# Optimization experiments

Measured on AMD Instinct MI355X. Metric: run time of the kernel, lower is better.

## Reference

```python
import jax, jax.numpy as jnp
import numpy as np

B, S, E, H = 8, 3072, 512, 8  # batch, total seq (3 chunks of 1024), emb_size, num_heads


def setup_inputs() -> dict:
    key = jax.random.key(0)
    ks = jax.random.split(key, 9)
    sc = 0.02  # weight init scale
    return {
        "x": jax.random.normal(ks[0], (B, S, E), jnp.float32),
        "Wq": jax.random.normal(ks[1], (3, E, E), jnp.float32) * sc,
        "bq": jax.random.normal(ks[2], (3, E), jnp.float32) * sc,
        "Wk": jax.random.normal(ks[3], (3, E, E), jnp.float32) * sc,
        "bk": jax.random.normal(ks[4], (3, E), jnp.float32) * sc,
        "Wv": jax.random.normal(ks[5], (3, E, E), jnp.float32) * sc,
        "bv": jax.random.normal(ks[6], (3, E), jnp.float32) * sc,
        "Wp": jax.random.normal(ks[7], (3, E, E), jnp.float32) * sc,
        "bp": jax.random.normal(ks[8], (3, E), jnp.float32) * sc,
    }


def reference(x, Wq, bq, Wk, bk, Wv, bv, Wp, bp):
    b, s, e = x.shape
    d = e // H
    # split into 3 chunks along seq: xc[c] is chunk c, shape [b, n, e]
    xc = jnp.stack(jnp.split(x, 3, axis=1))  # [3, b, n, e]

    def lin(W, bias):  # torch Linear: x @ W.T + b, per chunk
        return jnp.einsum('cbne,cfe->cbnf', xc, W) + bias[:, None, None, :]

    def heads(t):  # [3, b, n, e] -> [3, b, h, n, d]
        c, bb, n, _ = t.shape
        return t.reshape(c, bb, n, H, d).transpose(0, 1, 3, 2, 4)

    q = heads(lin(Wq, bq))
    k = heads(lin(Wk, bk))
    v = heads(lin(Wv, bv))

    # rotated cross-chunk pairing (faithful to source):
    # out1 = attn(q2, k3, v3); out2 = attn(q3, k1, v1); out3 = attn(q1, k2, v2)
    q_sel = q[jnp.array([1, 2, 0])]
    k_sel = k[jnp.array([2, 0, 1])]
    v_sel = v[jnp.array([2, 0, 1])]

    scaling = jnp.sqrt(jnp.float32(e))  # note: sqrt(emb_size), not sqrt(head_dim)
    energy = jnp.einsum('cbhqd,cbhkd->cbhqk', q_sel, k_sel) / scaling
    att = jax.nn.softmax(energy, axis=-1)  # dropout: eval-mode identity
    out = jnp.einsum('cbhqk,cbhkd->cbhqd', att, v_sel)
    out = out.transpose(0, 1, 3, 2, 4).reshape(3, b, s // 3, e)  # merge heads
    out = jnp.einsum('cbne,cfe->cbnf', out, Wp) + bp[:, None, None, :]
    return jnp.concatenate([out[0], out[1], out[2]], axis=1)  # [b, s, e]
```

## Files before the change

### kernel.cpp

```cpp
#include <hip/hip_runtime.h>
#include <hip/hip_bf16.h>


typedef __attribute__((ext_vector_type(8))) short short8v;
typedef __attribute__((ext_vector_type(4))) float float4v;
typedef __attribute__((ext_vector_type(4))) unsigned short ushort4v;
typedef __attribute__((ext_vector_type(4))) unsigned int uint4v;

#define CHUNKS 3
#define BATCH 8
#define SEQ 3072
#define EMB 512
#define NH 8
#define HD 64
#define NCK 1024
#define MTOT (BATCH*SEQ)
#define QKV_ELEMS (CHUNKS*BATCH*NH*NCK*HD)
#define WELEMS (CHUNKS*EMB*EMB)
#define QSCALE 0.06375872465f

__device__ __forceinline__ unsigned short f2b(float f) {
  union { float f; unsigned int i; } x; x.f = f;
  unsigned int r = x.i + 0x7FFFu + ((x.i >> 16) & 1u);
  return (unsigned short)(r >> 16);
}
__device__ __forceinline__ unsigned int pack2r(float a, float b) {
  union { float f; unsigned int u; } xa, xb; xa.f = a; xb.f = b;
  return __builtin_amdgcn_perm(xb.u + 0x8000u, xa.u + 0x8000u, 0x07060302u);
}
__device__ __forceinline__ void gld_lds16(const unsigned short* g, unsigned short* l) {
  __builtin_amdgcn_global_load_lds(
      (const __attribute__((address_space(1))) unsigned int*)g,
      (__attribute__((address_space(3))) unsigned int*)l, 16, 0, 0);
}
#define MFMA(a, b, c) __builtin_amdgcn_mfma_f32_16x16x32_bf16(a, b, c, 0, 0, 0)

__global__ __launch_bounds__(256) void conv_x(
    const float* __restrict__ src, unsigned short* __restrict__ dst)
{
  size_t i = ((size_t)blockIdx.x * 256 + threadIdx.x) * 8;
  float4 a = *(const float4*)&src[i];
  float4 b = *(const float4*)&src[i + 4];
  uint4v p;
  p[0] = pack2r(a.x, a.y); p[1] = pack2r(a.z, a.w);
  p[2] = pack2r(b.x, b.y); p[3] = pack2r(b.z, b.w);
  *(uint4v*)&dst[i] = p;
}

__global__ __launch_bounds__(256) void conv_w(
    const float* __restrict__ s0, const float* __restrict__ s1,
    const float* __restrict__ s2, const float* __restrict__ s3,
    unsigned short* __restrict__ dst)
{
  const int z = blockIdx.y;
  const float* s = (z == 0) ? s0 : (z == 1) ? s1 : (z == 2) ? s2 : s3;
  size_t i = ((size_t)blockIdx.x * 256 + threadIdx.x) * 8;
  float4 a = *(const float4*)&s[i];
  float4 b = *(const float4*)&s[i + 4];
  uint4v p;
  p[0] = pack2r(a.x, a.y); p[1] = pack2r(a.z, a.w);
  p[2] = pack2r(b.x, b.y); p[3] = pack2r(b.z, b.w);
  *(uint4v*)&dst[(size_t)z * WELEMS + i] = p;
}

__global__ __launch_bounds__(256) void qkv_gemm(
    const unsigned short* __restrict__ xb, const unsigned short* __restrict__ Wb,
    const float* __restrict__ bq, const float* __restrict__ bk,
    const float* __restrict__ bv,
    unsigned short* __restrict__ qt, unsigned short* __restrict__ kt,
    unsigned short* __restrict__ vt)
{
  const int tid = threadIdx.x;
  const int w = tid >> 6, l = tid & 63;
  const int ln = l & 15, qu = l >> 4;
  const int sr = l >> 3, kbl = l & 7;
  const int bid = blockIdx.x;
  const int lin = (bid & 7) * 288 + (bid >> 3);
  const int col0 = (lin & 3) * 128;
  const int z = (lin >> 2) % 3;
  const int row0 = (lin / 12) * 128;
  const int bglob = row0 / SEQ;
  const int c = (row0 % SEQ) / NCK;
  const int n0 = row0 % NCK;
  const unsigned short* W = Wb + (size_t)z * WELEMS + c * EMB * EMB;
  const float* bias = (z == 0 ? bq : (z == 1 ? bk : bv)) + c * EMB;
  const float oscale = (z == 0) ? QSCALE : 1.0f;

  __shared__ unsigned short As[128 * 64];
  __shared__ unsigned short Bs[128 * 64];

  const int xo = (w & 1) * 64, fo = (w >> 1) * 64;

  float4v acc[4][4];
#pragma unroll
  for (int i = 0; i < 4; ++i)
#pragma unroll
    for (int j = 0; j < 4; ++j) acc[i][j] = (float4v){0.f, 0.f, 0.f, 0.f};

  for (int k0 = 0; k0 < EMB; k0 += 64) {
    __syncthreads();
#pragma unroll
    for (int s = 0; s < 4; ++s) {
      int rbase = w * 32 + s * 8;
      int r = rbase + sr;
      int kb_g = kbl ^ sr;
      gld_lds16(&xb[(size_t)(row0 + r) * EMB + k0 + kb_g * 8], &As[rbase * 64]);
      gld_lds16(&W [(size_t)(col0 + r) * EMB + k0 + kb_g * 8], &Bs[rbase * 64]);
    }
    __syncthreads();
#pragma unroll
    for (int ks = 0; ks < 2; ++ks) {
      short8v xf[4], wf[4];
#pragma unroll
      for (int i = 0; i < 4; ++i) {
        int rx = xo + 16 * i + ln;
        xf[i] = *(const short8v*)&As[rx * 64 + (((ks * 4 + qu) ^ (rx & 7)) * 8)];
        int rw = fo + 16 * i + ln;
        wf[i] = *(const short8v*)&Bs[rw * 64 + (((ks * 4 + qu) ^ (rw & 7)) * 8)];
      }
      if (z <= 1) {
#pragma unroll
        for (int i = 0; i < 4; ++i)
#pragma unroll
          for (int j = 0; j < 4; ++j) acc[i][j] = MFMA(wf[j], xf[i], acc[i][j]);
      } else {
#pragma unroll
        for (int i = 0; i < 4; ++i)
#pragma unroll
          for (int j = 0; j < 4; ++j) acc[i][j] = MFMA(xf[i], wf[j], acc[i][j]);
      }
    }
  }

  if (z <= 1) {
    unsigned short* outp = (z == 0) ? qt : kt;
#pragma unroll
    for (int j = 0; j < 4; ++j) {
      int f0 = col0 + fo + 16 * j + 4 * qu;
      float4 b4 = *(const float4*)&bias[f0];
      int hh = f0 >> 6, dd0 = f0 & 63;
      size_t base = ((size_t)((c * 8 + bglob) * 8 + hh)) << 16;
#pragma unroll
      for (int i = 0; i < 4; ++i) {
        int n = n0 + xo + 16 * i + ln;
        ushort4v p;
#pragma unroll
        for (int r = 0; r < 4; ++r)
          p[r] = f2b((acc[i][j][r] + ((const float*)&b4)[r]) * oscale);
        *(ushort4v*)&outp[base + (size_t)n * 64 + dd0] = p;
      }
    }
  } else {
#pragma unroll
    for (int i = 0; i < 4; ++i) {
      int nn0 = n0 + xo + 16 * i + 4 * qu;
#pragma unroll
      for (int j = 0; j < 4; ++j) {
        int f = col0 + fo + 16 * j + ln;
        int hh = f >> 6, dd = f & 63;
        float bvv = bias[f];
        size_t base = ((size_t)((c * 8 + bglob) * 8 + hh)) << 16;
        ushort4v p;
#pragma unroll
        for (int r = 0; r < 4; ++r) p[r] = f2b(acc[i][j][r] + bvv);
        *(ushort4v*)&vt[base + (size_t)dd * 1024 + nn0] = p;
      }
    }
  }
}

#define ATTN_STAGE(buf, kt0v) do {                                             \
  int r = w * 8;                                                               \
  gld_lds16(&Kg[(size_t)((kt0v) + r + sr) * 64 + ((kbl ^ sr) * 8)],            \
            &Ks[buf][r * 64]);                                                 \
  gld_lds16(&Vg[(size_t)(r + sr) * 1024 + (kt0v) + ((kbl ^ sr) * 8)],          \
            &Vs[buf][r * 64]);                                                 \
} while (0)

__global__ __launch_bounds__(512) void attn_kernel(
    const unsigned short* __restrict__ qt,
    const unsigned short* __restrict__ kt,
    const unsigned short* __restrict__ vt,
    unsigned short* __restrict__ attnb)
{
  const int tid = threadIdx.x;
  const int w = tid >> 6, l = tid & 63;
  const int ln = l & 15, qu = l >> 4;
  const int sr = l >> 3, kbl = l & 7;
  const int bid = blockIdx.x;
  const int hd = bid % 192;
  const int q0 = (bid / 192) * 256;
  const int co = hd >> 6;
  const int b  = (hd >> 3) & 7;
  const int h  = hd & 7;
  const int cq = (co + 1) % 3, ckv = (co + 2) % 3;
  const unsigned short* Qg = qt + ((size_t)((cq  * 8 + b) * 8 + h) << 16);
  const unsigned short* Kg = kt + ((size_t)((ckv * 8 + b) * 8 + h) << 16);
  const unsigned short* Vg = vt + ((size_t)((ckv * 8 + b) * 8 + h) << 16);

  __shared__ unsigned short Ks[2][64 * 64];
  __shared__ unsigned short Vs[2][64 * 64];

  short8v qf[2][2];
#pragma unroll
  for (int nt = 0; nt < 2; ++nt)
#pragma unroll
    for (int ks = 0; ks < 2; ++ks)
      qf[nt][ks] = *(const short8v*)&Qg[(size_t)(q0 + w * 32 + nt * 16 + ln) * 64 + ks * 32 + qu * 8];

  short8v onesf;
#pragma unroll
  for (int i = 0; i < 8; ++i) onesf[i] = (short)0x3F80;

  float4v acc_o[4][2];
#pragma unroll
  for (int i = 0; i < 4; ++i)
#pragma unroll
    for (int j = 0; j < 2; ++j) acc_o[i][j] = (float4v){0.f, 0.f, 0.f, 0.f};
  float4v acc_l[2];
  acc_l[0] = (float4v){0.f, 0.f, 0.f, 0.f};
  acc_l[1] = (float4v){0.f, 0.f, 0.f, 0.f};

  ATTN_STAGE(0, 0);
  __syncthreads();
  int cur = 0;
  for (int kt0 = 0; kt0 < NCK; kt0 += 64) {
    if (kt0 + 64 < NCK) ATTN_STAGE(cur ^ 1, kt0 + 64);

    float4v sacc[4][2];
#pragma unroll
    for (int mt = 0; mt < 4; ++mt)
#pragma unroll
      for (int nt = 0; nt < 2; ++nt) sacc[mt][nt] = (float4v){0.f, 0.f, 0.f, 0.f};
    __builtin_amdgcn_s_setprio(1);
#pragma unroll
    for (int ks = 0; ks < 2; ++ks) {
#pragma unroll
      for (int mt = 0; mt < 4; ++mt) {
        int key = 16 * mt + ln;
        short8v kf = *(const short8v*)&Ks[cur][key * 64 + (((ks * 4 + qu) ^ (key & 7)) * 8)];
#pragma unroll
        for (int nt = 0; nt < 2; ++nt)
          sacc[mt][nt] = MFMA(kf, qf[nt][ks], sacc[mt][nt]);
      }
    }
    __builtin_amdgcn_s_setprio(0);

#pragma unroll
    for (int ks2 = 0; ks2 < 2; ++ks2) {
      short8v pf[2];
#pragma unroll
      for (int nt = 0; nt < 2; ++nt) {
        float4v s0v = sacc[2 * ks2][nt];
        float4v s1v = sacc[2 * ks2 + 1][nt];
        float a0 = __builtin_amdgcn_exp2f(s0v[0]);
        float a1 = __builtin_amdgcn_exp2f(s0v[1]);
        float a2 = __builtin_amdgcn_exp2f(s0v[2]);
        float a3 = __builtin_amdgcn_exp2f(s0v[3]);
        float b0 = __builtin_amdgcn_exp2f(s1v[0]);
        float b1 = __builtin_amdgcn_exp2f(s1v[1]);
        float b2 = __builtin_amdgcn_exp2f(s1v[2]);
        float b3 = __builtin_amdgcn_exp2f(s1v[3]);
        unsigned int m00 = pack2r(a0, a1);
        unsigned int m01 = pack2r(a2, a3);
        unsigned int m10 = pack2r(b0, b1);
        unsigned int m11 = pack2r(b2, b3);
        asm("v_permlane32_swap_b32 %0, %1" : "+v"(m00), "+v"(m10));
        asm("v_permlane32_swap_b32 %0, %1" : "+v"(m01), "+v"(m11));
        asm("v_permlane16_swap_b32 %0, %1" : "+v"(m00), "+v"(m10));
        asm("v_permlane16_swap_b32 %0, %1" : "+v"(m01), "+v"(m11));
        uint4v t; t[0] = m00; t[1] = m01; t[2] = m10; t[3] = m11;
        pf[nt] = __builtin_bit_cast(short8v, t);
      }
      __builtin_amdgcn_s_setprio(1);
#pragma unroll
      for (int nt = 0; nt < 2; ++nt)
        acc_l[nt] = MFMA(onesf, pf[nt], acc_l[nt]);
#pragma unroll
      for (int mt2 = 0; mt2 < 4; ++mt2) {
        int dd = 16 * mt2 + ln;
        short8v vf = *(const short8v*)&Vs[cur][dd * 64 + (((ks2 * 4 + qu) ^ (dd & 7)) * 8)];
#pragma unroll
        for (int nt = 0; nt < 2; ++nt)
          acc_o[mt2][nt] = MFMA(vf, pf[nt], acc_o[mt2][nt]);
      }
      __builtin_amdgcn_s_setprio(0);
    }

    __syncthreads();
    cur ^= 1;
  }

  float inv[2];
  inv[0] = 1.0f / acc_l[0][0];
  inv[1] = 1.0f / acc_l[1][0];
  unsigned short* Og = attnb + (size_t)((co * 8 + b)) * NCK * EMB + h * HD;
#pragma unroll
  for (int mt = 0; mt < 4; ++mt) {
    int dd0 = 16 * mt + 4 * qu;
#pragma unroll
    for (int nt = 0; nt < 2; ++nt) {
      int q_glob = q0 + w * 32 + nt * 16 + ln;
      ushort4v p;
#pragma unroll
      for (int r = 0; r < 4; ++r) p[r] = f2b(acc_o[mt][nt][r] * inv[nt]);
      *(ushort4v*)&Og[(size_t)q_glob * EMB + dd0] = p;
    }
  }
}

__global__ __launch_bounds__(256) void proj_gemm(
    const unsigned short* __restrict__ attnb,
    const unsigned short* __restrict__ Wpb, const float* __restrict__ bp,
    float* __restrict__ out)
{
  const int tid = threadIdx.x;
  const int w = tid >> 6, l = tid & 63;
  const int ln = l & 15, qu = l >> 4;
  const int sr = l >> 3, kbl = l & 7;
  const int bid = blockIdx.x;
  const int lin = (bid & 7) * 96 + (bid >> 3);
  const int col0 = (lin & 3) * 128;
  const int row0 = (lin >> 2) * 128;
  const int c = row0 >> 13;
  const int bglob = (row0 >> 10) & 7;
  const int n0 = row0 & 1023;
  const unsigned short* W = Wpb + c * EMB * EMB;
  const float* bias = bp + c * EMB;

  __shared__ unsigned short As[128 * 64];
  __shared__ unsigned short Bs[128 * 64];

  const int xo = (w & 1) * 64, fo = (w >> 1) * 64;

  float4v acc[4][4];
#pragma unroll
  for (int i = 0; i < 4; ++i)
#pragma unroll
    for (int j = 0; j < 4; ++j) acc[i][j] = (float4v){0.f, 0.f, 0.f, 0.f};

  for (int k0 = 0; k0 < EMB; k0 += 64) {
    __syncthreads();
#pragma unroll
    for (int s = 0; s < 4; ++s) {
      int rbase = w * 32 + s * 8;
      int r = rbase + sr;
      int kb_g = kbl ^ sr;
      gld_lds16(&attnb[(size_t)(row0 + r) * EMB + k0 + kb_g * 8], &As[rbase * 64]);
      gld_lds16(&W    [(size_t)(col0 + r) * EMB + k0 + kb_g * 8], &Bs[rbase * 64]);
    }
    __syncthreads();
#pragma unroll
    for (int ks = 0; ks < 2; ++ks) {
      short8v xf[4], wf[4];
#pragma unroll
      for (int i = 0; i < 4; ++i) {
        int rx = xo + 16 * i + ln;
        xf[i] = *(const short8v*)&As[rx * 64 + (((ks * 4 + qu) ^ (rx & 7)) * 8)];
        int rw = fo + 16 * i + ln;
        wf[i] = *(const short8v*)&Bs[rw * 64 + (((ks * 4 + qu) ^ (rw & 7)) * 8)];
      }
#pragma unroll
      for (int i = 0; i < 4; ++i)
#pragma unroll
        for (int j = 0; j < 4; ++j) acc[i][j] = MFMA(wf[j], xf[i], acc[i][j]);
    }
  }

#pragma unroll
  for (int j = 0; j < 4; ++j) {
    int f0 = col0 + fo + 16 * j + 4 * qu;
    float4 b4 = *(const float4*)&bias[f0];
#pragma unroll
    for (int i = 0; i < 4; ++i) {
      int srow = bglob * SEQ + c * NCK + n0 + xo + 16 * i + ln;
      float4 o;
      o.x = acc[i][j][0] + b4.x;
      o.y = acc[i][j][1] + b4.y;
      o.z = acc[i][j][2] + b4.z;
      o.w = acc[i][j][3] + b4.w;
      *(float4*)&out[(size_t)srow * EMB + f0] = o;
    }
  }
}

extern "C" void kernel_launch(void* const* d_in, const int* in_sizes, int n_in,
                              void* d_out, int out_size, void* d_ws, size_t ws_size,
                              hipStream_t stream) {
  (void)in_sizes; (void)n_in; (void)out_size; (void)ws_size;
  const float* x  = (const float*)d_in[0];
  const float* Wq = (const float*)d_in[1];
  const float* bq = (const float*)d_in[2];
  const float* Wk = (const float*)d_in[3];
  const float* bk = (const float*)d_in[4];
  const float* Wv = (const float*)d_in[5];
  const float* bv = (const float*)d_in[6];
  const float* Wp = (const float*)d_in[7];
  const float* bp = (const float*)d_in[8];
  float* out = (float*)d_out;

  unsigned short* Wb   = (unsigned short*)d_ws;
  unsigned short* qt   = Wb + 4 * (size_t)WELEMS;
  unsigned short* kt   = qt + QKV_ELEMS;
  unsigned short* vt   = kt + QKV_ELEMS;
  unsigned short* attn = vt + QKV_ELEMS;
  unsigned short* xbf  = attn;

  conv_x<<<QKV_ELEMS / (256 * 8), 256, 0, stream>>>(x, xbf);
  conv_w<<<dim3(WELEMS / (256 * 8), 4), 256, 0, stream>>>(Wq, Wk, Wv, Wp, Wb);
  qkv_gemm<<<(MTOT / 128) * (EMB / 128) * 3, 256, 0, stream>>>(
      xbf, Wb, bq, bk, bv, qt, kt, vt);
  attn_kernel<<<(NCK / 256) * CHUNKS * BATCH * NH, 512, 0, stream>>>(qt, kt, vt, attn);
  proj_gemm<<<(MTOT / 128) * (EMB / 128), 256, 0, stream>>>(attn, Wb + 3 * (size_t)WELEMS, bp, out);
}
```

Before: 267.1 us.

## Load 128-key K/V tiles per sync instead of double-buffered 64-key tiles

Drops the double-buffered prefetch pipeline in the attention kernel. Each iteration now loads a 128-key block of K and V into shared memory between two barriers, then processes it as two 64-key sub-tiles. The first QK MFMA of each sub-tile uses a zero constant accumulator instead of explicit zero-init. This halves the number of barrier rounds but removes the overlap of global loads with compute, so load latency is exposed unless other blocks on the same CU hide it.

```diff
diff --git a/kernel.cpp b/kernel.cpp
--- a/kernel.cpp
+++ b/kernel.cpp
@@ -169,14 +169,6 @@
   }
 }
 
-#define ATTN_STAGE(buf, kt0v) do {                                             \
-  int r = w * 8;                                                               \
-  gld_lds16(&Kg[(size_t)((kt0v) + r + sr) * 64 + ((kbl ^ sr) * 8)],            \
-            &Ks[buf][r * 64]);                                                 \
-  gld_lds16(&Vg[(size_t)(r + sr) * 1024 + (kt0v) + ((kbl ^ sr) * 8)],          \
-            &Vs[buf][r * 64]);                                                 \
-} while (0)
-
 __global__ __launch_bounds__(512) void attn_kernel(
     const unsigned short* __restrict__ qt,
     const unsigned short* __restrict__ kt,
@@ -198,7 +190,7 @@
   const unsigned short* Kg = kt + ((size_t)((ckv * 8 + b) * 8 + h) << 16);
   const unsigned short* Vg = vt + ((size_t)((ckv * 8 + b) * 8 + h) << 16);
 
-  __shared__ unsigned short Ks[2][64 * 64];
+  __shared__ unsigned short Ks[128 * 64];
   __shared__ unsigned short Vs[2][64 * 64];
 
   short8v qf[2][2];
@@ -211,6 +203,7 @@
   short8v onesf;
 #pragma unroll
   for (int i = 0; i < 8; ++i) onesf[i] = (short)0x3F80;
+  const float4v zf = (float4v){0.f, 0.f, 0.f, 0.f};
 
   float4v acc_o[4][2];
 #pragma unroll
@@ -218,77 +211,88 @@
 #pragma unroll
     for (int j = 0; j < 2; ++j) acc_o[i][j] = (float4v){0.f, 0.f, 0.f, 0.f};
   float4v acc_l[2];
-  acc_l[0] = (float4v){0.f, 0.f, 0.f, 0.f};
-  acc_l[1] = (float4v){0.f, 0.f, 0.f, 0.f};
-
-  ATTN_STAGE(0, 0);
-  __syncthreads();
-  int cur = 0;
-  for (int kt0 = 0; kt0 < NCK; kt0 += 64) {
-    if (kt0 + 64 < NCK) ATTN_STAGE(cur ^ 1, kt0 + 64);
-
-    float4v sacc[4][2];
-#pragma unroll
-    for (int mt = 0; mt < 4; ++mt)
-#pragma unroll
-      for (int nt = 0; nt < 2; ++nt) sacc[mt][nt] = (float4v){0.f, 0.f, 0.f, 0.f};
-    __builtin_amdgcn_s_setprio(1);
-#pragma unroll
-    for (int ks = 0; ks < 2; ++ks) {
+  acc_l[0] = zf;
+  acc_l[1] = zf;
+
+  for (int kt0 = 0; kt0 < NCK; kt0 += 128) {
+    __syncthreads();
+    {
+      int rK = w * 16;
+      gld_lds16(&Kg[(size_t)(kt0 + rK + sr) * 64 + ((kbl ^ sr) * 8)],
+                &Ks[rK * 64]);
+      gld_lds16(&Kg[(size_t)(kt0 + rK + 8 + sr) * 64 + ((kbl ^ sr) * 8)],
+                &Ks[(rK + 8) * 64]);
+      int rV = w * 8;
+      gld_lds16(&Vg[(size_t)(rV + sr) * 1024 + kt0 + ((kbl ^ sr) * 8)],
+                &Vs[0][rV * 64]);
+      gld_lds16(&Vg[(size_t)(rV + sr) * 1024 + kt0 + 64 + ((kbl ^ sr) * 8)],
+                &Vs[1][rV * 64]);
+    }
+    __syncthreads();
+
+#pragma unroll
+    for (int sub = 0; sub < 2; ++sub) {
+      const int sub64 = sub * 64;
+
+      float4v sacc[4][2];
+      __builtin_amdgcn_s_setprio(1);
 #pragma unroll
       for (int mt = 0; mt < 4; ++mt) {
-        int key = 16 * mt + ln;
-        short8v kf = *(const short8v*)&Ks[cur][key * 64 + (((ks * 4 + qu) ^ (key & 7)) * 8)];
+        int key = sub64 + 16 * mt + ln;
+        short8v kf = *(const short8v*)&Ks[key * 64 + ((qu ^ (key & 7)) * 8)];
+        sacc[mt][0] = MFMA(kf, qf[0][0], zf);
+        sacc[mt][1] = MFMA(kf, qf[1][0], zf);
+      }
+#pragma unroll
+      for (int mt = 0; mt < 4; ++mt) {
+        int key = sub64 + 16 * mt + ln;
+        short8v kf = *(const short8v*)&Ks[key * 64 + (((4 + qu) ^ (key & 7)) * 8)];
+        sacc[mt][0] = MFMA(kf, qf[0][1], sacc[mt][0]);
+        sacc[mt][1] = MFMA(kf, qf[1][1], sacc[mt][1]);
+      }
+      __builtin_amdgcn_s_setprio(0);
+
+#pragma unroll
+      for (int ks2 = 0; ks2 < 2; ++ks2) {
+        short8v pf[2];
+#pragma unroll
+        for (int nt = 0; nt < 2; ++nt) {
+          float4v s0v = sacc[2 * ks2][nt];
+          float4v s1v = sacc[2 * ks2 + 1][nt];
+          float a0 = __builtin_amdgcn_exp2f(s0v[0]);
+          float a1 = __builtin_amdgcn_exp2f(s0v[1]);
+          float a2 = __builtin_amdgcn_exp2f(s0v[2]);
+          float a3 = __builtin_amdgcn_exp2f(s0v[3]);
+          float b0 = __builtin_amdgcn_exp2f(s1v[0]);
+          float b1 = __builtin_amdgcn_exp2f(s1v[1]);
+          float b2 = __builtin_amdgcn_exp2f(s1v[2]);
+          float b3 = __builtin_amdgcn_exp2f(s1v[3]);
+          unsigned int m00 = pack2r(a0, a1);
+          unsigned int m01 = pack2r(a2, a3);
+          unsigned int m10 = pack2r(b0, b1);
+          unsigned int m11 = pack2r(b2, b3);
+          asm("v_permlane32_swap_b32 %0, %1" : "+v"(m00), "+v"(m10));
+          asm("v_permlane32_swap_b32 %0, %1" : "+v"(m01), "+v"(m11));
+          asm("v_permlane16_swap_b32 %0, %1" : "+v"(m00), "+v"(m10));
+          asm("v_permlane16_swap_b32 %0, %1" : "+v"(m01), "+v"(m11));
+          uint4v t; t[0] = m00; t[1] = m01; t[2] = m10; t[3] = m11;
+          pf[nt] = __builtin_bit_cast(short8v, t);
+        }
+        __builtin_amdgcn_s_setprio(1);
 #pragma unroll
         for (int nt = 0; nt < 2; ++nt)
-          sacc[mt][nt] = MFMA(kf, qf[nt][ks], sacc[mt][nt]);
-      }
-    }
-    __builtin_amdgcn_s_setprio(0);
-
-#pragma unroll
-    for (int ks2 = 0; ks2 < 2; ++ks2) {
-      short8v pf[2];
-#pragma unroll
-      for (int nt = 0; nt < 2; ++nt) {
-        float4v s0v = sacc[2 * ks2][nt];
-        float4v s1v = sacc[2 * ks2 + 1][nt];
-        float a0 = __builtin_amdgcn_exp2f(s0v[0]);
-        float a1 = __builtin_amdgcn_exp2f(s0v[1]);
-        float a2 = __builtin_amdgcn_exp2f(s0v[2]);
-        float a3 = __builtin_amdgcn_exp2f(s0v[3]);
-        float b0 = __builtin_amdgcn_exp2f(s1v[0]);
-        float b1 = __builtin_amdgcn_exp2f(s1v[1]);
-        float b2 = __builtin_amdgcn_exp2f(s1v[2]);
-        float b3 = __builtin_amdgcn_exp2f(s1v[3]);
-        unsigned int m00 = pack2r(a0, a1);
-        unsigned int m01 = pack2r(a2, a3);
-        unsigned int m10 = pack2r(b0, b1);
-        unsigned int m11 = pack2r(b2, b3);
-        asm("v_permlane32_swap_b32 %0, %1" : "+v"(m00), "+v"(m10));
-        asm("v_permlane32_swap_b32 %0, %1" : "+v"(m01), "+v"(m11));
-        asm("v_permlane16_swap_b32 %0, %1" : "+v"(m00), "+v"(m10));
-        asm("v_permlane16_swap_b32 %0, %1" : "+v"(m01), "+v"(m11));
-        uint4v t; t[0] = m00; t[1] = m01; t[2] = m10; t[3] = m11;
-        pf[nt] = __builtin_bit_cast(short8v, t);
-      }
-      __builtin_amdgcn_s_setprio(1);
-#pragma unroll
-      for (int nt = 0; nt < 2; ++nt)
-        acc_l[nt] = MFMA(onesf, pf[nt], acc_l[nt]);
-#pragma unroll
-      for (int mt2 = 0; mt2 < 4; ++mt2) {
-        int dd = 16 * mt2 + ln;
-        short8v vf = *(const short8v*)&Vs[cur][dd * 64 + (((ks2 * 4 + qu) ^ (dd & 7)) * 8)];
-#pragma unroll
-        for (int nt = 0; nt < 2; ++nt)
-          acc_o[mt2][nt] = MFMA(vf, pf[nt], acc_o[mt2][nt]);
-      }
-      __builtin_amdgcn_s_setprio(0);
-    }
-
-    __syncthreads();
-    cur ^= 1;
+          acc_l[nt] = MFMA(onesf, pf[nt], acc_l[nt]);
+#pragma unroll
+        for (int mt2 = 0; mt2 < 4; ++mt2) {
+          int dd = 16 * mt2 + ln;
+          short8v vf = *(const short8v*)&Vs[sub][dd * 64 + (((ks2 * 4 + qu) ^ (dd & 7)) * 8)];
+#pragma unroll
+          for (int nt = 0; nt < 2; ++nt)
+            acc_o[mt2][nt] = MFMA(vf, pf[nt], acc_o[mt2][nt]);
+        }
+        __builtin_amdgcn_s_setprio(0);
+      }
+    }
   }
 
   float inv[2];
```

New measurement: 256.0 us. 4.2% less time.
